# Kernel tuning notes

Measured on AMD Instinct MI355X. Metric: run time of the kernel, lower is better.

Reference implementation:

```python
import jax, jax.numpy as jnp
import numpy as np

N = 131072          # total rows across all types
IN_C = 512          # in_channels
OUT_C = 512         # out_channels
NUM_TYPES = 8       # len(types)


def setup_inputs() -> dict:
    key = jax.random.key(0)
    k1, k2, k3, k4 = jax.random.split(key, 4)
    x = jax.random.normal(k1, (N, IN_C), dtype=jnp.float32)
    type_vec = jnp.sort(jax.random.randint(k2, (N,), 0, NUM_TYPES)).astype(jnp.int64)
    # HeteroLinear params: weight [num_types, in, out], bias [num_types, out]
    scale = 1.0 / np.sqrt(IN_C)
    weight = jax.random.normal(k3, (NUM_TYPES, IN_C, OUT_C), dtype=jnp.float32) * scale
    bias = jax.random.normal(k4, (NUM_TYPES, OUT_C), dtype=jnp.float32) * scale
    return {"x": x, "type_vec": type_vec, "weight": weight, "bias": bias}


def _grouped_linear(x, type_vec, weight, bias):
    """out[n] = x[n] @ weight[type_vec[n]] + bias[type_vec[n]].

    Computed as T masked dense GEMMs (T is small) to avoid gathering a
    [N, in, out] per-row weight tensor.
    """
    n, out_c = x.shape[0], weight.shape[2]

    def per_type(acc, t):
        mask = (type_vec == t).astype(x.dtype)[:, None]  # [N, 1]
        y = (x * mask) @ weight[t] + mask * bias[t]      # [N, out]
        return acc + y, None

    out, _ = jax.lax.scan(per_type,
                          jnp.zeros((n, out_c), dtype=x.dtype),
                          jnp.arange(weight.shape[0]))
    return out


def reference(x, type_vec, weight, bias):
    # Equivalent to ToHeteroLinear.fused_forward (and dict_forward after the
    # cat/repeat_interleave, since type_vec is sorted / is_sorted=True).
    return _grouped_linear(x, type_vec, weight, bias)
```

## Files before the change

kernel.cpp:

```cpp
#include <hip/hip_runtime.h>

#define NROWS 131072
#define KDIM 512
#define NDIM 512

using short8  = __attribute__((ext_vector_type(8))) short;
using float4v = __attribute__((ext_vector_type(4))) float;
using uint4v  = __attribute__((ext_vector_type(4))) unsigned int;

__device__ __forceinline__ unsigned pack_trunc(float a, float b) {
    unsigned ua = __builtin_bit_cast(unsigned, a);
    unsigned ub = __builtin_bit_cast(unsigned, b);
    return __builtin_amdgcn_perm(ub, ua, 0x07060302u);
}
__device__ __forceinline__ unsigned pack_round(float a, float b) {
    unsigned ua = __builtin_bit_cast(unsigned, a) + 0x8000u;
    unsigned ub = __builtin_bit_cast(unsigned, b) + 0x8000u;
    return __builtin_amdgcn_perm(ub, ua, 0x07060302u);
}

__device__ __forceinline__ void glds16(const void* g, void* l) {
    __builtin_amdgcn_global_load_lds(
        (__attribute__((address_space(1))) void*)g,
        (__attribute__((address_space(3))) void*)l, 16, 0, 0);
}

__global__ __launch_bounds__(256) void prep_kernel(const float* __restrict__ w,
                                                   unsigned short* __restrict__ wt,
                                                   const float* __restrict__ x,
                                                   unsigned short* __restrict__ xb) {
    __shared__ float tile[64][65];
    if (blockIdx.x < 512) {
        int b  = blockIdx.x;
        int ty = b >> 6;
        int ot = (b >> 3) & 7;
        int it = b & 7;
        const float* wp = w + ((size_t)ty << 18);
        int tid = threadIdx.x;
        int cf = tid & 15, ir0 = tid >> 4;
        #pragma unroll
        for (int j = 0; j < 4; ++j) {
            int ir = ir0 + 16 * j;
            float4v v = *(const float4v*)(wp + (size_t)(it * 64 + ir) * NDIM + ot * 64 + cf * 4);
            tile[ir][cf * 4 + 0] = v.x;
            tile[ir][cf * 4 + 1] = v.y;
            tile[ir][cf * 4 + 2] = v.z;
            tile[ir][cf * 4 + 3] = v.w;
        }
        __syncthreads();
        int oc = tid >> 2, iq = tid & 3;
        unsigned* op = (unsigned*)(wt + ((size_t)ty << 18) + (size_t)(ot * 64 + oc) * KDIM + it * 64 + iq * 16);
        #pragma unroll
        for (int j = 0; j < 8; ++j)
            op[j] = pack_round(tile[iq * 16 + 2 * j][oc], tile[iq * 16 + 2 * j + 1][oc]);
    } else {
        const size_t total = (size_t)NROWS * KDIM / 8;
        size_t i = (size_t)(blockIdx.x - 512) * 256 + threadIdx.x;
        const size_t stride = (size_t)2048 * 256;
        const float4v* xv = (const float4v*)x;
        uint4v* ov = (uint4v*)xb;
        for (; i < total; i += stride) {
            float4v a = __builtin_nontemporal_load(&xv[2 * i]);
            float4v c = __builtin_nontemporal_load(&xv[2 * i + 1]);
            uint4v o;
            o.x = pack_round(a.x, a.y);
            o.y = pack_round(a.z, a.w);
            o.z = pack_round(c.x, c.y);
            o.w = pack_round(c.z, c.w);
            ov[i] = o;
        }
    }
}

__global__ __launch_bounds__(256, 2)
void hetero_gemm_pre(const unsigned short* __restrict__ xb,
                     const int* __restrict__ tv,
                     const unsigned short* __restrict__ wt,
                     const float* __restrict__ bias,
                     float* __restrict__ out) {
    __shared__ uint4v ldsA[4][4 * 128];
    __shared__ uint4v ldsB[4][4 * 128];

    const int b = blockIdx.x;
    const int rowTile = ((b >> 5) << 3) | (b & 7);
    const int colTile = (b >> 3) & 3;
    const int row0 = rowTile << 7;
    const int col0 = colTile << 7;

    const int tid  = threadIdx.x;
    const int lane = tid & 63;
    const int wave = tid >> 6;
    const int wm   = (wave & 1) << 6;
    const int wn   = (wave >> 1) << 6;
    const int l15  = lane & 15;
    const int quad = lane >> 4;

    const int i128 = tid & 127;
    const int g2   = tid >> 7;

    const int t0 = tv[row0];
    const int t1 = tv[row0 + 127];

    const unsigned short* abase = xb + (size_t)(row0 + i128) * KDIM + g2 * 8;

    for (int tt = t0; tt <= t1; ++tt) {
        const unsigned short* wbase =
            wt + ((size_t)tt << 18) + (size_t)(col0 + i128) * KDIM + g2 * 8;

        float4v acc[4][4];
        float4v zero = {0.f, 0.f, 0.f, 0.f};
        #pragma unroll
        for (int i = 0; i < 4; ++i)
            #pragma unroll
            for (int j = 0; j < 4; ++j)
                acc[i][j] = zero;

#define STAGE(c, bufi)                                                       \
    do {                                                                     \
        glds16(abase + (c) * 32,      &ldsA[bufi][ g2      * 128 + i128]);   \
        glds16(abase + (c) * 32 + 16, &ldsA[bufi][(g2 + 2) * 128 + i128]);   \
        glds16(wbase + (c) * 32,      &ldsB[bufi][ g2      * 128 + i128]);   \
        glds16(wbase + (c) * 32 + 16, &ldsB[bufi][(g2 + 2) * 128 + i128]);   \
    } while (0)

        STAGE(0, 0);
        STAGE(1, 1);
        STAGE(2, 2);

        #pragma unroll
        for (int k = 0; k < 16; ++k) {
            if (k < 14)       asm volatile("s_waitcnt vmcnt(8)" ::: "memory");
            else if (k == 14) asm volatile("s_waitcnt vmcnt(4)" ::: "memory");
            else              asm volatile("s_waitcnt vmcnt(0)" ::: "memory");
            __builtin_amdgcn_s_barrier();

            const int cur = k & 3;

            if (k + 3 < 16) STAGE(k + 3, (k + 3) & 3);

            short8 af[4], bf[4];
            #pragma unroll
            for (int mi = 0; mi < 4; ++mi)
                af[mi] = *(const short8*)&ldsA[cur][quad * 128 + wm + mi * 16 + l15];
            #pragma unroll
            for (int ni = 0; ni < 4; ++ni)
                bf[ni] = *(const short8*)&ldsB[cur][quad * 128 + wn + ni * 16 + l15];

            #pragma unroll
            for (int mi = 0; mi < 4; ++mi)
                #pragma unroll
                for (int ni = 0; ni < 4; ++ni)
                    acc[mi][ni] = __builtin_amdgcn_mfma_f32_16x16x32_bf16(
                        af[mi], bf[ni], acc[mi][ni], 0, 0, 0);
        }
#undef STAGE

        float bcol[4];
        #pragma unroll
        for (int ni = 0; ni < 4; ++ni)
            bcol[ni] = bias[(size_t)tt * NDIM + col0 + wn + ni * 16 + l15];

        #pragma unroll
        for (int mi = 0; mi < 4; ++mi) {
            #pragma unroll
            for (int r = 0; r < 4; ++r) {
                const int grow = row0 + wm + mi * 16 + quad * 4 + r;
                if (tv[grow] == tt) {
                    float* orow = out + (size_t)grow * NDIM;
                    #pragma unroll
                    for (int ni = 0; ni < 4; ++ni) {
                        const int gcol = col0 + wn + ni * 16 + l15;
                        orow[gcol] = acc[mi][ni][r] + bcol[ni];
                    }
                }
            }
        }
    }
}

__global__ __launch_bounds__(256, 2)
void hetero_gemm_fallback(const float* __restrict__ x,
                          const int* __restrict__ tv,
                          const unsigned short* __restrict__ wt,
                          const float* __restrict__ bias,
                          float* __restrict__ out) {
    __shared__ uint4v ldsA[4 * 128];
    __shared__ uint4v ldsB[4 * 128];

    const int b = blockIdx.x;
    const int rowTile = ((b >> 5) << 3) | (b & 7);
    const int colTile = (b >> 3) & 3;
    const int row0 = rowTile << 7;
    const int col0 = colTile << 7;

    const int tid  = threadIdx.x;
    const int lane = tid & 63;
    const int wave = tid >> 6;
    const int wm   = (wave & 1) << 6;
    const int wn   = (wave >> 1) << 6;
    const int l15  = lane & 15;
    const int quad = lane >> 4;

    const int ra = tid >> 1;
    const int khalf = tid & 1;
    const int rtypeA = tv[row0 + ra];

    const int nb = tid & 127;
    const int g2 = tid >> 7;

    const int t0 = tv[row0];
    const int t1 = tv[row0 + 127];

    float4v acc[4][4];
    float4v zero = {0.f, 0.f, 0.f, 0.f};
    #pragma unroll
    for (int i = 0; i < 4; ++i)
        #pragma unroll
        for (int j = 0; j < 4; ++j)
            acc[i][j] = zero;

    for (int tt = t0; tt <= t1; ++tt) {
        const unsigned maskA = (rtypeA == tt) ? 0xFFFFFFFFu : 0u;
        const float* ap = x + (size_t)(row0 + ra) * KDIM + khalf * 16;
        const unsigned short* wb = wt + ((size_t)tt << 18) + (size_t)(col0 + nb) * KDIM;

        float4v av[4];
        uint4v  bv[2];
        #pragma unroll
        for (int i = 0; i < 4; ++i) av[i] = *(const float4v*)(ap + i * 4);
        bv[0] = *(const uint4v*)(wb + g2 * 8);
        bv[1] = *(const uint4v*)(wb + (g2 + 2) * 8);

        for (int kc = 0; kc < KDIM; kc += 32) {
            __syncthreads();
            uint4v pa0, pa1;
            pa0.x = pack_trunc(av[0].x, av[0].y) & maskA;
            pa0.y = pack_trunc(av[0].z, av[0].w) & maskA;
            pa0.z = pack_trunc(av[1].x, av[1].y) & maskA;
            pa0.w = pack_trunc(av[1].z, av[1].w) & maskA;
            pa1.x = pack_trunc(av[2].x, av[2].y) & maskA;
            pa1.y = pack_trunc(av[2].z, av[2].w) & maskA;
            pa1.z = pack_trunc(av[3].x, av[3].y) & maskA;
            pa1.w = pack_trunc(av[3].z, av[3].w) & maskA;
            ldsA[(khalf * 2 + 0) * 128 + ra] = pa0;
            ldsA[(khalf * 2 + 1) * 128 + ra] = pa1;
            ldsB[(g2    ) * 128 + nb] = bv[0];
            ldsB[(g2 + 2) * 128 + nb] = bv[1];
            __syncthreads();

            if (kc + 32 < KDIM) {
                const float* ap2 = ap + kc + 32;
                #pragma unroll
                for (int i = 0; i < 4; ++i) av[i] = *(const float4v*)(ap2 + i * 4);
                const unsigned short* wb2 = wb + kc + 32;
                bv[0] = *(const uint4v*)(wb2 + g2 * 8);
                bv[1] = *(const uint4v*)(wb2 + (g2 + 2) * 8);
            }

            short8 af[4], bf[4];
            #pragma unroll
            for (int mi = 0; mi < 4; ++mi)
                af[mi] = *(const short8*)&ldsA[quad * 128 + wm + mi * 16 + l15];
            #pragma unroll
            for (int ni = 0; ni < 4; ++ni)
                bf[ni] = *(const short8*)&ldsB[quad * 128 + wn + ni * 16 + l15];
            #pragma unroll
            for (int mi = 0; mi < 4; ++mi)
                #pragma unroll
                for (int ni = 0; ni < 4; ++ni)
                    acc[mi][ni] = __builtin_amdgcn_mfma_f32_16x16x32_bf16(
                        af[mi], bf[ni], acc[mi][ni], 0, 0, 0);
        }
    }

    #pragma unroll
    for (int mi = 0; mi < 4; ++mi) {
        #pragma unroll
        for (int r = 0; r < 4; ++r) {
            const int grow = row0 + wm + mi * 16 + quad * 4 + r;
            const int rt = tv[grow];
            const float* brow = bias + (size_t)rt * NDIM;
            float* orow = out + (size_t)grow * NDIM;
            #pragma unroll
            for (int ni = 0; ni < 4; ++ni) {
                const int gcol = col0 + wn + ni * 16 + l15;
                orow[gcol] = acc[mi][ni][r] + brow[gcol];
            }
        }
    }
}

extern "C" void kernel_launch(void* const* d_in, const int* in_sizes, int n_in,
                              void* d_out, int out_size, void* d_ws, size_t ws_size,
                              hipStream_t stream) {
    const float* x    = (const float*)d_in[0];
    const int*   tv   = (const int*)d_in[1];
    const float* w    = (const float*)d_in[2];
    const float* bias = (const float*)d_in[3];
    float* out = (float*)d_out;

    unsigned short* wtr = (unsigned short*)d_ws;
    const size_t WTN  = (size_t)8 * 512 * 512;
    const size_t NEED = WTN * 2 + (size_t)NROWS * KDIM * 2;

    if (ws_size >= NEED) {
        unsigned short* xb = wtr + WTN;
        prep_kernel<<<2560, 256, 0, stream>>>(w, wtr, x, xb);
        hetero_gemm_pre<<<4096, 256, 0, stream>>>(xb, tv, wtr, bias, out);
    } else {
        prep_kernel<<<512, 256, 0, stream>>>(w, wtr, x, nullptr);
        hetero_gemm_fallback<<<4096, 256, 0, stream>>>(x, tv, wtr, bias, out);
    }
}
```

Baseline: 604.7 us.

## Replace 128x128 GEMM tiles with 256x256 tiles and an 8-wave phased pipeline

Replaces the 128x128 per-block grouped GEMM with a 256x256 tile computed by 512 threads (8 waves, each owning a 128x64 sub-tile). The K loop now uses 64-wide chunks, double-buffered in LDS, and interleaves global-to-LDS loads with MFMA phases using barriers, s_setprio and sched_barrier. Blocks are remapped so that neighbouring column tiles share the same row panel. The goal is higher arithmetic intensity and less global/L2 traffic per FLOP. In exchange it raises register and LDS use, drops occupancy to one block per CU, and wastes more work on tiles that straddle type boundaries.

```diff
diff --git a/kernel.cpp b/kernel.cpp
--- a/kernel.cpp
+++ b/kernel.cpp
@@ -72,110 +72,193 @@
     }
 }
 
-__global__ __launch_bounds__(256, 2)
-void hetero_gemm_pre(const unsigned short* __restrict__ xb,
+__global__ __launch_bounds__(512, 1)
+void hetero_gemm_256(const unsigned short* __restrict__ xb,
                      const int* __restrict__ tv,
                      const unsigned short* __restrict__ wt,
                      const float* __restrict__ bias,
                      float* __restrict__ out) {
-    __shared__ uint4v ldsA[4][4 * 128];
-    __shared__ uint4v ldsB[4][4 * 128];
-
-    const int b = blockIdx.x;
-    const int rowTile = ((b >> 5) << 3) | (b & 7);
-    const int colTile = (b >> 3) & 3;
-    const int row0 = rowTile << 7;
-    const int col0 = colTile << 7;
+    __shared__ uint4v lds[2][4][1024];
+
+    const int bhw = blockIdx.x;
+    const int b = (bhw & 7) * 128 + (bhw >> 3);
+    const int rowTile = b >> 1;
+    const int colTile = b & 1;
+    const int row0 = rowTile << 8;
+    const int col0 = colTile << 8;
 
     const int tid  = threadIdx.x;
     const int lane = tid & 63;
-    const int wave = tid >> 6;
-    const int wm   = (wave & 1) << 6;
-    const int wn   = (wave >> 1) << 6;
+    const int wid  = tid >> 6;
+    const int wr   = wid >> 2;
+    const int wc   = wid & 3;
     const int l15  = lane & 15;
     const int quad = lane >> 4;
-
-    const int i128 = tid & 127;
-    const int g2   = tid >> 7;
+    const int segB  = 2 + (wc >> 1);
+    const int cbase = (wc & 1) * 64;
 
     const int t0 = tv[row0];
-    const int t1 = tv[row0 + 127];
-
-    const unsigned short* abase = xb + (size_t)(row0 + i128) * KDIM + g2 * 8;
+    const int t1 = tv[row0 + 255];
+
+    const unsigned short* aPanel = xb + (size_t)row0 * KDIM;
+
+#define RD_A(SL, H)                                                           \
+    do {                                                                      \
+        _Pragma("unroll")                                                     \
+        for (int kk = 0; kk < 2; ++kk)                                        \
+            _Pragma("unroll")                                                 \
+            for (int j = 0; j < 4; ++j)                                       \
+                afr[kk][j] = *(const short8*)&lds[SL][wr]                     \
+                    [(kk * 4 + quad) * 128 + (H) * 64 + j * 16 + l15];        \
+    } while (0)
+
+#define RD_B(SL, V)                                                           \
+    do {                                                                      \
+        _Pragma("unroll")                                                     \
+        for (int kk = 0; kk < 2; ++kk)                                        \
+            _Pragma("unroll")                                                 \
+            for (int i = 0; i < 2; ++i)                                       \
+                bfr[kk][(V) * 2 + i] = *(const short8*)&lds[SL][segB]         \
+                    [(kk * 4 + quad) * 128 + cbase + ((V) * 2 + i) * 16 + l15]; \
+    } while (0)
+
+#define MMA(H, V)                                                             \
+    do {                                                                      \
+        __builtin_amdgcn_s_setprio(1);                                        \
+        _Pragma("unroll")                                                     \
+        for (int j = 0; j < 4; ++j)                                           \
+            _Pragma("unroll")                                                 \
+            for (int i = 0; i < 2; ++i)                                       \
+                _Pragma("unroll")                                             \
+                for (int kk = 0; kk < 2; ++kk)                                \
+                    acc[(H) * 4 + j][(V) * 2 + i] =                           \
+                        __builtin_amdgcn_mfma_f32_16x16x32_bf16(              \
+                            afr[kk][j], bfr[kk][(V) * 2 + i],                 \
+                            acc[(H) * 4 + j][(V) * 2 + i], 0, 0, 0);          \
+        __builtin_amdgcn_s_setprio(0);                                        \
+    } while (0)
+
+#define ST_A(SL, H, KT)                                                       \
+    do {                                                                      \
+        const unsigned short* g_ = aPanel +                                   \
+            (size_t)((H) * 128 + (tid & 127)) * KDIM + (KT) * 64 + (tid >> 7) * 8; \
+        glds16(g_,      &lds[SL][H][tid]);                                    \
+        glds16(g_ + 32, &lds[SL][H][tid + 512]);                              \
+    } while (0)
+
+#define ST_B(SL, G, KT)                                                       \
+    do {                                                                      \
+        const unsigned short* g_ = wPanel +                                   \
+            (size_t)((G) * 128 + (tid & 127)) * KDIM + (KT) * 64 + (tid >> 7) * 8; \
+        glds16(g_,      &lds[SL][2 + (G)][tid]);                              \
+        glds16(g_ + 32, &lds[SL][2 + (G)][tid + 512]);                        \
+    } while (0)
+
+#define BAR()  __builtin_amdgcn_s_barrier()
+#define PH_SYNC()                                                             \
+    do {                                                                      \
+        __builtin_amdgcn_s_barrier();                                         \
+        asm volatile("s_waitcnt lgkmcnt(0)" ::: "memory");                    \
+        __builtin_amdgcn_sched_barrier(0);                                    \
+    } while (0)
+#define VMW4() asm volatile("s_waitcnt vmcnt(4)" ::: "memory")
+#define VMW0() asm volatile("s_waitcnt vmcnt(0)" ::: "memory")
 
     for (int tt = t0; tt <= t1; ++tt) {
-        const unsigned short* wbase =
-            wt + ((size_t)tt << 18) + (size_t)(col0 + i128) * KDIM + g2 * 8;
-
-        float4v acc[4][4];
+        const unsigned short* wPanel = wt + ((size_t)tt << 18) + (size_t)col0 * KDIM;
+
+        float4v acc[8][4];
         float4v zero = {0.f, 0.f, 0.f, 0.f};
         #pragma unroll
-        for (int i = 0; i < 4; ++i)
-            #pragma unroll
-            for (int j = 0; j < 4; ++j)
-                acc[i][j] = zero;
-
-#define STAGE(c, bufi)                                                       \
-    do {                                                                     \
-        glds16(abase + (c) * 32,      &ldsA[bufi][ g2      * 128 + i128]);   \
-        glds16(abase + (c) * 32 + 16, &ldsA[bufi][(g2 + 2) * 128 + i128]);   \
-        glds16(wbase + (c) * 32,      &ldsB[bufi][ g2      * 128 + i128]);   \
-        glds16(wbase + (c) * 32 + 16, &ldsB[bufi][(g2 + 2) * 128 + i128]);   \
-    } while (0)
-
-        STAGE(0, 0);
-        STAGE(1, 1);
-        STAGE(2, 2);
-
-        #pragma unroll
-        for (int k = 0; k < 16; ++k) {
-            if (k < 14)       asm volatile("s_waitcnt vmcnt(8)" ::: "memory");
-            else if (k == 14) asm volatile("s_waitcnt vmcnt(4)" ::: "memory");
-            else              asm volatile("s_waitcnt vmcnt(0)" ::: "memory");
-            __builtin_amdgcn_s_barrier();
-
-            const int cur = k & 3;
-
-            if (k + 3 < 16) STAGE(k + 3, (k + 3) & 3);
-
-            short8 af[4], bf[4];
-            #pragma unroll
-            for (int mi = 0; mi < 4; ++mi)
-                af[mi] = *(const short8*)&ldsA[cur][quad * 128 + wm + mi * 16 + l15];
+        for (int mi = 0; mi < 8; ++mi)
             #pragma unroll
             for (int ni = 0; ni < 4; ++ni)
-                bf[ni] = *(const short8*)&ldsB[cur][quad * 128 + wn + ni * 16 + l15];
-
-            #pragma unroll
-            for (int mi = 0; mi < 4; ++mi)
-                #pragma unroll
-                for (int ni = 0; ni < 4; ++ni)
-                    acc[mi][ni] = __builtin_amdgcn_mfma_f32_16x16x32_bf16(
-                        af[mi], bf[ni], acc[mi][ni], 0, 0, 0);
-        }
-#undef STAGE
+                acc[mi][ni] = zero;
+
+        short8 afr[2][4];
+        short8 bfr[2][4];
+
+        ST_B(0, 0, 0); ST_B(0, 1, 0);
+        ST_A(0, 0, 0); ST_A(0, 1, 0);
+        ST_B(1, 0, 1); ST_B(1, 1, 1);
+        VMW4();
+        BAR();
+
+        #pragma unroll
+        for (int it = 0; it < 4; ++it) {
+            const int kt = it * 2;
+            RD_A(0, 0); RD_B(0, 0);
+            ST_A(1, 0, kt + 1);
+            PH_SYNC();
+            MMA(0, 0);
+            BAR();
+            RD_B(0, 1);
+            ST_A(1, 1, kt + 1);
+            PH_SYNC();
+            MMA(0, 1);
+            BAR();
+            RD_A(0, 1);
+            if (it < 3) ST_B(0, 0, kt + 2);
+            PH_SYNC();
+            MMA(1, 1);
+            BAR();
+            if (it < 3) ST_B(0, 1, kt + 2);
+            BAR();
+            MMA(1, 0);
+            if (it < 3) { VMW4(); } else { VMW0(); }
+            BAR();
+            RD_A(1, 0); RD_B(1, 0);
+            if (it < 3) ST_A(0, 0, kt + 2);
+            PH_SYNC();
+            MMA(0, 0);
+            BAR();
+            RD_B(1, 1);
+            if (it < 3) ST_A(0, 1, kt + 2);
+            PH_SYNC();
+            MMA(0, 1);
+            BAR();
+            RD_A(1, 1);
+            if (it < 3) ST_B(1, 0, kt + 3);
+            PH_SYNC();
+            MMA(1, 1);
+            BAR();
+            if (it < 3) ST_B(1, 1, kt + 3);
+            BAR();
+            MMA(1, 0);
+            if (it < 3) { VMW4(); } else { VMW0(); }
+            BAR();
+        }
 
         float bcol[4];
         #pragma unroll
         for (int ni = 0; ni < 4; ++ni)
-            bcol[ni] = bias[(size_t)tt * NDIM + col0 + wn + ni * 16 + l15];
-
-        #pragma unroll
-        for (int mi = 0; mi < 4; ++mi) {
+            bcol[ni] = bias[(size_t)tt * NDIM + col0 + wc * 64 + ni * 16 + l15];
+
+        #pragma unroll
+        for (int mi = 0; mi < 8; ++mi) {
             #pragma unroll
             for (int r = 0; r < 4; ++r) {
-                const int grow = row0 + wm + mi * 16 + quad * 4 + r;
+                const int grow = row0 + wr * 128 + mi * 16 + quad * 4 + r;
                 if (tv[grow] == tt) {
                     float* orow = out + (size_t)grow * NDIM;
                     #pragma unroll
                     for (int ni = 0; ni < 4; ++ni) {
-                        const int gcol = col0 + wn + ni * 16 + l15;
+                        const int gcol = col0 + wc * 64 + ni * 16 + l15;
                         orow[gcol] = acc[mi][ni][r] + bcol[ni];
                     }
                 }
             }
         }
     }
+#undef RD_A
+#undef RD_B
+#undef MMA
+#undef ST_A
+#undef ST_B
+#undef BAR
+#undef PH_SYNC
+#undef VMW4
+#undef VMW0
 }
 
 __global__ __launch_bounds__(256, 2)
@@ -306,7 +389,7 @@
     if (ws_size >= NEED) {
         unsigned short* xb = wtr + WTN;
         prep_kernel<<<2560, 256, 0, stream>>>(w, wtr, x, xb);
-        hetero_gemm_pre<<<4096, 256, 0, stream>>>(xb, tv, wtr, bias, out);
+        hetero_gemm_256<<<1024, 512, 0, stream>>>(xb, tv, wtr, bias, out);
     } else {
         prep_kernel<<<512, 256, 0, stream>>>(w, wtr, x, nullptr);
         hetero_gemm_fallback<<<4096, 256, 0, stream>>>(x, tv, wtr, bias, out);
```

Result: slower. 705.4 us (+16.6%).
